# Performance work log

Measured on AMD Instinct MI355X. Metric: run time of the kernel, lower is better.

The kernel has to match this reference:

```python
import jax, jax.numpy as jnp
import numpy as np

KSIZE = 11
SIGMA = 1.5
PAD = KSIZE // 2
C1 = 0.01 ** 2
C2 = 0.03 ** 2


def gaussian_kernel(ksize, sigma):
    ax = np.arange(ksize, dtype=np.float32) - (ksize - 1) / 2.0
    g = np.exp(-(ax ** 2) / (2.0 * sigma ** 2))
    k2d = np.outer(g, g)
    k2d = k2d / k2d.sum()
    # depthwise kernel for 3 channels: [out=3, in/groups=1, kh, kw]
    return jnp.asarray(np.broadcast_to(k2d, (3, 1, ksize, ksize)).copy())


def dwconv(x, kernel):
    # x: [B,3,H,W], kernel: [3,1,k,k], 'same' padding, groups=3
    return jax.lax.conv_general_dilated(
        x, kernel,
        window_strides=(1, 1),
        padding=[(PAD, PAD), (PAD, PAD)],
        dimension_numbers=('NCHW', 'OIHW', 'NCHW'),
        feature_group_count=3)


def setup_inputs() -> dict:
    key = jax.random.key(0)
    k1, k2 = jax.random.split(key)
    shape = (16, 3, 512, 512)
    img_output = jax.random.uniform(k1, shape, dtype=jnp.float32)
    img_target = jax.random.uniform(k2, shape, dtype=jnp.float32)
    kernel = gaussian_kernel(KSIZE, SIGMA)
    return {"img_output": img_output, "img_target": img_target, "kernel": kernel}


def reference(img_output, img_target, kernel):
    s, t = img_output, img_target
    ux = dwconv(s, kernel)
    uy = dwconv(t, kernel)
    uxx = dwconv(s * s, kernel)
    uyy = dwconv(t * t, kernel)
    uxy = dwconv(s * t, kernel)
    ssim = ((2 * ux * uy + C1) * (2 * (uxy - ux * uy) + C2)
            / (ux ** 2 + uy ** 2 + C1)
            / (uxx - ux * ux + (uyy - uy * uy) + C2))
    return 1.0 - ssim.mean()
```

## Files before the change

kernel.cpp:

```cpp
#include <hip/hip_runtime.h>
#include <stdint.h>

typedef _Float16 f16;
typedef f16  f16x8 __attribute__((ext_vector_type(8)));
typedef f16  f16x4 __attribute__((ext_vector_type(4)));
typedef f16  f16x2 __attribute__((ext_vector_type(2)));
typedef float f32x4 __attribute__((ext_vector_type(4)));

#define W 512
#define H 512
#define KS 11
#define NW 4
#define NBLK 3072
#define NLINES 256
#define C1_SSIM 0.0001f
#define C2_SSIM 0.0009f
#define NTOTAL 12582912.0f

#define LROWS 80
#define LCOLS 80
#define NCHUNK 50

__device__ __constant__ const float GW[KS] = {
    1.02838e-3f, 7.59876e-3f, 3.600076e-2f, 1.0936069e-1f, 2.1300554e-1f,
    2.6601172e-1f,
    2.1300554e-1f, 1.0936069e-1f, 3.600076e-2f, 7.59876e-3f, 1.02838e-3f
};

__device__ inline float ssim_px(float ux, float uy, float uxx, float uyy, float uxy) {
    const float uxuy = ux * uy;
    const float a = 2.f * uxuy + C1_SSIM;
    const float b = 2.f * (uxy - uxuy) + C2_SSIM;
    const float c = ux * ux + uy * uy + C1_SSIM;
    const float d = (uxx - ux * ux) + (uyy - uy * uy) + C2_SSIM;
    return (a * b) * __builtin_amdgcn_rcpf(c * d);
}

__device__ __forceinline__ f16x8 pack84(f32x4 a, f32x4 b) {
    f16x8 r;
    f16x2 h;
    h = __builtin_bit_cast(f16x2, __builtin_amdgcn_cvt_pkrtz(a[0], a[1]));
    r[0] = h[0]; r[1] = h[1];
    h = __builtin_bit_cast(f16x2, __builtin_amdgcn_cvt_pkrtz(a[2], a[3]));
    r[2] = h[0]; r[3] = h[1];
    h = __builtin_bit_cast(f16x2, __builtin_amdgcn_cvt_pkrtz(b[0], b[1]));
    r[4] = h[0]; r[5] = h[1];
    h = __builtin_bit_cast(f16x2, __builtin_amdgcn_cvt_pkrtz(b[2], b[3]));
    r[6] = h[0]; r[7] = h[1];
    return r;
}

__global__ __launch_bounds__(256, 3)
void ssim_main(const float* __restrict__ simg, const float* __restrict__ timg,
               float* __restrict__ accum, const float* __restrict__ zbuf) {
    __shared__ __align__(16) float lds[2][LROWS * LCOLS];
    __shared__ float red[NW];

    const int tid  = threadIdx.x;
    const int w    = tid >> 6;
    const int lane = tid & 63;
    const int n    = lane & 15;
    const int q    = lane >> 4;

    const int bid = blockIdx.x;
    const int z   = bid >> 6;
    const int rr  = bid & 63;
    const int ty  = rr >> 3;
    const int tx  = rr & 7;

    const float* sp = simg + ((size_t)z << 18);
    const float* tp = timg + ((size_t)z << 18);
    const int x0    = tx << 6;
    const int ybase = (ty << 6) - 5;
    const int xbase = x0 - 8;

    #pragma unroll
    for (int k = 0; k < 13; ++k) {
        const int c = (k << 2) + w;
        if (c < NCHUNK) {
            const int img  = (c >= 25) ? 1 : 0;
            const int cc   = img ? (c - 25) : c;
            const int off  = (cc << 10) + (lane << 4);
            const int t    = off >> 6;
            const int row  = (t * 205) >> 10;
            const int colb = off - row * 320;
            const int ry   = ybase + row;
            const int gcol = xbase + (colb >> 2);
            const float* src = img ? tp : sp;
            const bool ok = ((unsigned)ry < (unsigned)H) &
                            ((unsigned)gcol <= (unsigned)(W - 4));
            const float* ga = ok ? (src + ((size_t)ry << 9) + gcol) : zbuf;
            void* ldst = (char*)(&lds[0][0]) + (c << 10);
            __builtin_amdgcn_global_load_lds(
                (const uint32_t __attribute__((address_space(1)))*)ga,
                (uint32_t __attribute__((address_space(3)))*)ldst,
                16, 0, 0);
        }
    }

    f16x8 af;
    #pragma unroll
    for (int j = 0; j < 8; ++j) {
        const int k = (q << 3) + j;
        const int d = k - n - 3;
        af[j] = (d >= 0 && d < KS) ? (f16)GW[d] : (f16)0.f;
    }
    f16x4 a1v, a2v;
    #pragma unroll
    for (int j = 0; j < 4; ++j) {
        const int k  = (q << 2) + j;
        const int d1 = k - n;
        const int d2 = k + 16 - n;
        a1v[j] = (d1 >= 0 && d1 < KS) ? (f16)GW[d1] : (f16)0.f;
        a2v[j] = (d2 >= 0 && d2 < KS) ? (f16)GW[d2] : (f16)0.f;
    }

    __syncthreads();

    union H4 { f16x4 v4; f16x2 v2[2]; };
    const int coff = (w << 4) + (q << 3);
    const float* ls = &lds[0][coff];
    const float* lt = &lds[1][coff];

    f16x4 ph[2][5];
    float sum = 0.f;

    #pragma unroll
    for (int g = 0; g < 5; ++g) {
        const int ro = ((g << 4) + n) * LCOLS;
        const f32x4 s0 = *(const f32x4*)(ls + ro);
        const f32x4 s1 = *(const f32x4*)(ls + ro + 4);
        const f32x4 t0 = *(const f32x4*)(lt + ro);
        const f32x4 t1 = *(const f32x4*)(lt + ro + 4);
        const f16x8 sf = pack84(s0, s1);
        const f16x8 tf = pack84(t0, t1);
        const int pb = g & 1;
        #pragma unroll
        for (int c = 0; c < 5; ++c) {
            f16x8 ch;
            if      (c == 0) ch = sf;
            else if (c == 1) ch = tf;
            else if (c == 2) ch = sf * sf;
            else if (c == 3) ch = tf * tf;
            else             ch = sf * tf;
            const f32x4 zero = {0.f, 0.f, 0.f, 0.f};
            const f32x4 d = __builtin_amdgcn_mfma_f32_16x16x32_f16(ch, af, zero, 0, 0, 0);
            H4 u;
            u.v2[0] = __builtin_bit_cast(f16x2, __builtin_amdgcn_cvt_pkrtz(d[0], d[1]));
            u.v2[1] = __builtin_bit_cast(f16x2, __builtin_amdgcn_cvt_pkrtz(d[2], d[3]));
            ph[pb][c] = u.v4;
        }
        if (g >= 1) {
            const int pa = pb ^ 1;
            f32x4 acc[5];
            #pragma unroll
            for (int c = 0; c < 5; ++c) {
                const f32x4 zero = {0.f, 0.f, 0.f, 0.f};
                f32x4 a = __builtin_amdgcn_mfma_f32_16x16x16f16(a2v, ph[pb][c], zero, 0, 0, 0);
                a = __builtin_amdgcn_mfma_f32_16x16x16f16(a1v, ph[pa][c], a, 0, 0, 0);
                acc[c] = a;
            }
            #pragma unroll
            for (int rg = 0; rg < 4; ++rg)
                sum += ssim_px(acc[0][rg], acc[1][rg], acc[2][rg],
                               acc[3][rg], acc[4][rg]);
        }
    }

    #pragma unroll
    for (int off = 32; off > 0; off >>= 1)
        sum += __shfl_down(sum, off, 64);
    if (lane == 0) red[w] = sum;
    __syncthreads();
    if (tid == 0) {
        atomicAdd(&accum[(blockIdx.x & (NLINES - 1)) << 4],
                  red[0] + red[1] + red[2] + red[3]);
    }
}

__global__ void ssim_final(const float* __restrict__ accum, float* __restrict__ out) {
    const int lane = threadIdx.x;
    float s = 0.f;
    #pragma unroll
    for (int i = 0; i < NLINES / 64; ++i)
        s += accum[((i << 6) + lane) << 4];
    #pragma unroll
    for (int off = 32; off > 0; off >>= 1)
        s += __shfl_down(s, off, 64);
    if (lane == 0) out[0] = 1.f - s * (1.f / NTOTAL);
}

extern "C" void kernel_launch(void* const* d_in, const int* in_sizes, int n_in,
                              void* d_out, int out_size, void* d_ws, size_t ws_size,
                              hipStream_t stream) {
    const float* s = (const float*)d_in[0];
    const float* t = (const float*)d_in[1];
    float* out   = (float*)d_out;
    float* accum = (float*)d_ws;
    const float* zbuf = accum + NLINES * 16;

    hipMemsetAsync(accum, 0, NLINES * 16 * sizeof(float) + 256, stream);
    ssim_main<<<dim3(NBLK), 256, 0, stream>>>(s, t, accum, zbuf);
    ssim_final<<<1, 64, 0, stream>>>(accum, out);
}
```

Baseline: 138.5 us.

## Pipeline LDS tile loads by row group with staged vmcnt waits

Reorders the asynchronous global-to-LDS loads so that each 16-row group of both images is issued in turn. The single block-wide sync is replaced by per-group s_waitcnt vmcnt thresholds plus barriers, so MFMA work on early row groups can begin while later rows are still in flight. This is meant to hide load latency inside each block. It adds four extra barriers and relies on hand-counted vmcnt values that differ per wave, since waves 0-1 issue three loads per group and waves 2-3 issue two.

```diff
diff --git a/kernel.cpp b/kernel.cpp
--- a/kernel.cpp
+++ b/kernel.cpp
@@ -19,7 +19,6 @@
 
 #define LROWS 80
 #define LCOLS 80
-#define NCHUNK 50
 
 __device__ __constant__ const float GW[KS] = {
     1.02838e-3f, 7.59876e-3f, 3.600076e-2f, 1.0936069e-1f, 2.1300554e-1f,
@@ -50,6 +49,13 @@
     return r;
 }
 
+#define WAITG(N3, N2) do {                                            \
+    if (w < 2) asm volatile("s_waitcnt vmcnt(" #N3 ")" ::: "memory"); \
+    else       asm volatile("s_waitcnt vmcnt(" #N2 ")" ::: "memory"); \
+    __builtin_amdgcn_s_barrier();                                     \
+    __builtin_amdgcn_sched_barrier(0);                                \
+} while (0)
+
 __global__ __launch_bounds__(256, 3)
 void ssim_main(const float* __restrict__ simg, const float* __restrict__ timg,
                float* __restrict__ accum, const float* __restrict__ zbuf) {
@@ -75,27 +81,30 @@
     const int xbase = x0 - 8;
 
     #pragma unroll
-    for (int k = 0; k < 13; ++k) {
-        const int c = (k << 2) + w;
-        if (c < NCHUNK) {
-            const int img  = (c >= 25) ? 1 : 0;
-            const int cc   = img ? (c - 25) : c;
-            const int off  = (cc << 10) + (lane << 4);
-            const int t    = off >> 6;
-            const int row  = (t * 205) >> 10;
-            const int colb = off - row * 320;
-            const int ry   = ybase + row;
-            const int gcol = xbase + (colb >> 2);
-            const float* src = img ? tp : sp;
-            const bool ok = ((unsigned)ry < (unsigned)H) &
-                            ((unsigned)gcol <= (unsigned)(W - 4));
-            const float* ga = ok ? (src + ((size_t)ry << 9) + gcol) : zbuf;
-            void* ldst = (char*)(&lds[0][0]) + (c << 10);
-            __builtin_amdgcn_global_load_lds(
-                (const uint32_t __attribute__((address_space(1)))*)ga,
-                (uint32_t __attribute__((address_space(3)))*)ldst,
-                16, 0, 0);
+    for (int g = 0; g < 5; ++g) {
+        #pragma unroll
+        for (int k = 0; k < 3; ++k) {
+            const int c = w + (k << 2);
+            if (c < 10) {
+                const int img = (c >= 5) ? 1 : 0;
+                const int j   = img ? (c - 5) : c;
+                const int t   = (j << 6) + lane;
+                const int row = (t * 3277) >> 16;
+                const int cl  = t - row * 20;
+                const int ry   = ybase + (g << 4) + row;
+                const int gcol = xbase + (cl << 2);
+                const float* src = img ? tp : sp;
+                const bool ok = ((unsigned)ry < (unsigned)H) &
+                                ((unsigned)gcol <= (unsigned)(W - 4));
+                const float* ga = ok ? (src + ((size_t)ry << 9) + gcol) : zbuf;
+                void* ldst = (char*)(&lds[img][0]) + (g * 5120 + (j << 10));
+                __builtin_amdgcn_global_load_lds(
+                    (const uint32_t __attribute__((address_space(1)))*)ga,
+                    (uint32_t __attribute__((address_space(3)))*)ldst,
+                    16, 0, 0);
+            }
         }
+        __builtin_amdgcn_sched_barrier(0);
     }
 
     f16x8 af;
@@ -115,8 +124,6 @@
         a2v[j] = (d2 >= 0 && d2 < KS) ? (f16)GW[d2] : (f16)0.f;
     }
 
-    __syncthreads();
-
     union H4 { f16x4 v4; f16x2 v2[2]; };
     const int coff = (w << 4) + (q << 3);
     const float* ls = &lds[0][coff];
@@ -127,6 +134,12 @@
 
     #pragma unroll
     for (int g = 0; g < 5; ++g) {
+        if      (g == 0) WAITG(12, 8);
+        else if (g == 1) WAITG(9, 6);
+        else if (g == 2) WAITG(6, 4);
+        else if (g == 3) WAITG(3, 2);
+        else             WAITG(0, 0);
+
         const int ro = ((g << 4) + n) * LCOLS;
         const f32x4 s0 = *(const f32x4*)(ls + ro);
         const f32x4 s1 = *(const f32x4*)(ls + ro + 4);
```

After: 141.3 us. 2.0% more time.

## Make SSIM kernel persistent with double-buffered LDS DMA pipeline

Applied to the files above, without the earlier changes.

Replaces the 3072 one-tile blocks with 256 persistent 512-thread blocks, each looping over 12 tiles. The next tile's global-to-LDS DMA is issued while the current tile is computed, using two LDS buffers and explicit vmcnt waits. Each tile's rows are split between two groups of four waves, and per-block atomics become plain stores. This is meant to hide load latency and cut launch and tail overhead, at the cost of occupancy of only one block per CU and reliance on hand-set vmcnt counts.

```diff
diff --git a/kernel.cpp b/kernel.cpp
--- a/kernel.cpp
+++ b/kernel.cpp
@@ -10,16 +10,15 @@
 #define W 512
 #define H 512
 #define KS 11
-#define NW 4
-#define NBLK 3072
+#define NW 8
+#define NBLK 256
+#define NITER 12
 #define NLINES 256
 #define C1_SSIM 0.0001f
 #define C2_SSIM 0.0009f
 #define NTOTAL 12582912.0f
 
-#define LROWS 80
 #define LCOLS 80
-#define NCHUNK 50
 
 __device__ __constant__ const float GW[KS] = {
     1.02838e-3f, 7.59876e-3f, 3.600076e-2f, 1.0936069e-1f, 2.1300554e-1f,
@@ -50,83 +49,54 @@
     return r;
 }
 
-__global__ __launch_bounds__(256, 3)
-void ssim_main(const float* __restrict__ simg, const float* __restrict__ timg,
-               float* __restrict__ accum, const float* __restrict__ zbuf) {
-    __shared__ __align__(16) float lds[2][LROWS * LCOLS];
-    __shared__ float red[NW];
-
-    const int tid  = threadIdx.x;
-    const int w    = tid >> 6;
-    const int lane = tid & 63;
-    const int n    = lane & 15;
-    const int q    = lane >> 4;
-
-    const int bid = blockIdx.x;
-    const int z   = bid >> 6;
-    const int rr  = bid & 63;
-    const int ty  = rr >> 3;
-    const int tx  = rr & 7;
-
+__device__ __forceinline__ void issue_dma(const float* __restrict__ simg,
+                                          const float* __restrict__ timg,
+                                          const float* __restrict__ zb,
+                                          int w, int lane, int T, float* ldsbase) {
+    const int z  = T >> 6;
+    const int rr = T & 63;
+    const int ty = rr >> 3;
+    const int tx = rr & 7;
     const float* sp = simg + ((size_t)z << 18);
     const float* tp = timg + ((size_t)z << 18);
-    const int x0    = tx << 6;
     const int ybase = (ty << 6) - 5;
-    const int xbase = x0 - 8;
-
-    #pragma unroll
-    for (int k = 0; k < 13; ++k) {
-        const int c = (k << 2) + w;
-        if (c < NCHUNK) {
-            const int img  = (c >= 25) ? 1 : 0;
-            const int cc   = img ? (c - 25) : c;
-            const int off  = (cc << 10) + (lane << 4);
-            const int t    = off >> 6;
-            const int row  = (t * 205) >> 10;
+    const int xbase = (tx << 6) - 8;
+    #pragma unroll
+    for (int k = 0; k < 7; ++k) {
+        const int c = (k << 3) + w;
+        if (c < 50) {
+            const int img = (c >= 25) ? 1 : 0;
+            const int cc  = img ? (c - 25) : c;
+            const int off = (cc << 10) + (lane << 4);
+            const int t16 = off >> 6;
+            const int row = (t16 * 205) >> 10;
             const int colb = off - row * 320;
             const int ry   = ybase + row;
             const int gcol = xbase + (colb >> 2);
             const float* src = img ? tp : sp;
             const bool ok = ((unsigned)ry < (unsigned)H) &
                             ((unsigned)gcol <= (unsigned)(W - 4));
-            const float* ga = ok ? (src + ((size_t)ry << 9) + gcol) : zbuf;
-            void* ldst = (char*)(&lds[0][0]) + (c << 10);
+            const float* ga = ok ? (src + ((size_t)ry << 9) + gcol) : zb;
+            void* ldst = (char*)ldsbase + (c << 10);
             __builtin_amdgcn_global_load_lds(
                 (const uint32_t __attribute__((address_space(1)))*)ga,
                 (uint32_t __attribute__((address_space(3)))*)ldst,
                 16, 0, 0);
         }
     }
-
-    f16x8 af;
-    #pragma unroll
-    for (int j = 0; j < 8; ++j) {
-        const int k = (q << 3) + j;
-        const int d = k - n - 3;
-        af[j] = (d >= 0 && d < KS) ? (f16)GW[d] : (f16)0.f;
-    }
-    f16x4 a1v, a2v;
-    #pragma unroll
-    for (int j = 0; j < 4; ++j) {
-        const int k  = (q << 2) + j;
-        const int d1 = k - n;
-        const int d2 = k + 16 - n;
-        a1v[j] = (d1 >= 0 && d1 < KS) ? (f16)GW[d1] : (f16)0.f;
-        a2v[j] = (d2 >= 0 && d2 < KS) ? (f16)GW[d2] : (f16)0.f;
-    }
-
-    __syncthreads();
-
+}
+
+__device__ __forceinline__ float compute_half(const float* __restrict__ base,
+                                              int coff, int n, int h,
+                                              f16x8 af, f16x4 a1v, f16x4 a2v) {
     union H4 { f16x4 v4; f16x2 v2[2]; };
-    const int coff = (w << 4) + (q << 3);
-    const float* ls = &lds[0][coff];
-    const float* lt = &lds[1][coff];
-
+    const float* ls = base + coff;
+    const float* lt = base + 6400 + coff;
     f16x4 ph[2][5];
     float sum = 0.f;
-
-    #pragma unroll
-    for (int g = 0; g < 5; ++g) {
+    #pragma unroll
+    for (int j = 0; j < 3; ++j) {
+        const int g  = (h << 1) + j;
         const int ro = ((g << 4) + n) * LCOLS;
         const f32x4 s0 = *(const f32x4*)(ls + ro);
         const f32x4 s1 = *(const f32x4*)(ls + ro + 4);
@@ -134,7 +104,7 @@
         const f32x4 t1 = *(const f32x4*)(lt + ro + 4);
         const f16x8 sf = pack84(s0, s1);
         const f16x8 tf = pack84(t0, t1);
-        const int pb = g & 1;
+        const int pb = j & 1;
         #pragma unroll
         for (int c = 0; c < 5; ++c) {
             f16x8 ch;
@@ -150,7 +120,7 @@
             u.v2[1] = __builtin_bit_cast(f16x2, __builtin_amdgcn_cvt_pkrtz(d[2], d[3]));
             ph[pb][c] = u.v4;
         }
-        if (g >= 1) {
+        if (j >= 1) {
             const int pa = pb ^ 1;
             f32x4 acc[5];
             #pragma unroll
@@ -166,6 +136,64 @@
                                acc[3][rg], acc[4][rg]);
         }
     }
+    return sum;
+}
+
+__global__ __launch_bounds__(512, 1)
+void ssim_main(const float* __restrict__ simg, const float* __restrict__ timg,
+               float* __restrict__ accum, const float* __restrict__ zbuf) {
+    __shared__ __align__(16) float lds[2][2 * 6400];
+    __shared__ float red[NW];
+
+    const int tid  = threadIdx.x;
+    const int w    = tid >> 6;
+    const int lane = tid & 63;
+    const int n    = lane & 15;
+    const int q    = lane >> 4;
+    const int h    = w >> 2;
+    const int cw   = w & 3;
+    const int bid  = blockIdx.x;
+
+    issue_dma(simg, timg, zbuf, w, lane, bid, &lds[0][0]);
+    __builtin_amdgcn_sched_barrier(0);
+
+    f16x8 af;
+    #pragma unroll
+    for (int j = 0; j < 8; ++j) {
+        const int k = (q << 3) + j;
+        const int d = k - n - 3;
+        af[j] = (d >= 0 && d < KS) ? (f16)GW[d] : (f16)0.f;
+    }
+    f16x4 a1v, a2v;
+    #pragma unroll
+    for (int j = 0; j < 4; ++j) {
+        const int k  = (q << 2) + j;
+        const int d1 = k - n;
+        const int d2 = k + 16 - n;
+        a1v[j] = (d1 >= 0 && d1 < KS) ? (f16)GW[d1] : (f16)0.f;
+        a2v[j] = (d2 >= 0 && d2 < KS) ? (f16)GW[d2] : (f16)0.f;
+    }
+
+    const int coff = (cw << 4) + (q << 3);
+    float sum = 0.f;
+
+    for (int t = 0; t < NITER; ++t) {
+        if (t < NITER - 1) {
+            issue_dma(simg, timg, zbuf, w, lane, bid + ((t + 1) << 8),
+                      &lds[(t + 1) & 1][0]);
+            __builtin_amdgcn_sched_barrier(0);
+            asm volatile("s_waitcnt vmcnt(6)" ::: "memory");
+        } else {
+            asm volatile("s_waitcnt vmcnt(0)" ::: "memory");
+        }
+        __builtin_amdgcn_s_barrier();
+        __builtin_amdgcn_sched_barrier(0);
+
+        sum += compute_half(&lds[t & 1][0], coff, n, h, af, a1v, a2v);
+
+        __builtin_amdgcn_sched_barrier(0);
+        __builtin_amdgcn_s_barrier();
+    }
 
     #pragma unroll
     for (int off = 32; off > 0; off >>= 1)
@@ -173,8 +201,10 @@
     if (lane == 0) red[w] = sum;
     __syncthreads();
     if (tid == 0) {
-        atomicAdd(&accum[(blockIdx.x & (NLINES - 1)) << 4],
-                  red[0] + red[1] + red[2] + red[3]);
+        float bs = 0.f;
+        #pragma unroll
+        for (int i = 0; i < NW; ++i) bs += red[i];
+        accum[bid << 4] = bs;
     }
 }
 
@@ -200,6 +230,6 @@
     const float* zbuf = accum + NLINES * 16;
 
     hipMemsetAsync(accum, 0, NLINES * 16 * sizeof(float) + 256, stream);
-    ssim_main<<<dim3(NBLK), 256, 0, stream>>>(s, t, accum, zbuf);
+    ssim_main<<<dim3(NBLK), 512, 0, stream>>>(s, t, accum, zbuf);
     ssim_final<<<1, 64, 0, stream>>>(accum, out);
 }
```

Result: no change. 137.5 us (-0.7%).
